# Optimization experiments

Hardware: AMD Instinct MI355X
Metric: run time of the kernel (lower is better)

The kernel has to match this reference:

```python
import jax, jax.numpy as jnp
from jax import lax
import numpy as np

V, D_EMB, H, P, B, T = 32000, 512, 1024, 512, 32, 512
NUM_LAYERS = 2


def setup_inputs() -> dict:
    key = jax.random.key(0)
    ks = jax.random.split(key, 2 + NUM_LAYERS * 5)
    tokens = jax.random.randint(ks[0], (B, T), 0, V, dtype=jnp.int32)
    embed = jax.random.normal(ks[1], (V, D_EMB), dtype=jnp.float32) * 0.02
    inp = {"tokens": tokens, "embed": embed}
    in_dims = [D_EMB] + [P] * (NUM_LAYERS - 1)
    for l in range(NUM_LAYERS):
        kk = ks[2 + 5 * l: 7 + 5 * l]
        inp[f"Wx{l}"] = jax.random.normal(kk[0], (in_dims[l], 4 * H), dtype=jnp.float32) * 0.02
        inp[f"Wh{l}"] = jax.random.normal(kk[1], (H, 4 * H), dtype=jnp.float32) * 0.02
        inp[f"b{l}"] = jnp.zeros((4 * H,), dtype=jnp.float32)
        inp[f"Wfc{l}"] = jax.random.normal(kk[3], (H, P), dtype=jnp.float32) * 0.02
        inp[f"bfc{l}"] = jnp.zeros((P,), dtype=jnp.float32)
    return inp


def _lstm(x, Wx, Wh, b):
    # x: [B, T, D] -> [B, T, H]. Keras gate order: i, f, g(cell), o.
    Bsz = x.shape[0]
    h0 = jnp.zeros((Bsz, H), dtype=x.dtype)
    c0 = jnp.zeros((Bsz, H), dtype=x.dtype)

    # Precompute input projection for all timesteps (one big GEMM).
    xz = jnp.einsum('btd,dg->btg', x, Wx) + b  # [B, T, 4H]

    def step(carry, zt):
        h, c = carry
        z = zt + h @ Wh
        i, f, g, o = jnp.split(z, 4, axis=-1)
        c = jax.nn.sigmoid(f) * c + jax.nn.sigmoid(i) * jnp.tanh(g)
        h = jax.nn.sigmoid(o) * jnp.tanh(c)
        return (h, c), h

    _, ys = lax.scan(step, (h0, c0), jnp.swapaxes(xz, 0, 1))  # ys: [T, B, H]
    return jnp.swapaxes(ys, 0, 1)


def reference(tokens, embed, Wx0, Wh0, b0, Wfc0, bfc0, Wx1, Wh1, b1, Wfc1, bfc1):
    # inference path: dropout is identity (training=False), use_softmax=False
    x = embed[tokens]  # [B, T, D_EMB]
    layers = [(Wx0, Wh0, b0, Wfc0, bfc0), (Wx1, Wh1, b1, Wfc1, bfc1)]
    for Wx, Wh, b, Wfc, bfc in layers:
        x = _lstm(x, Wx, Wh, b)
        x = x @ Wfc + bfc  # per-layer dense projection [B, T, P]
    return x
```

## Files before the change

### kernel.cpp

```cpp
#include <hip/hip_runtime.h>
#include <cstdio>
#include <cstdint>

typedef unsigned short u16;
typedef unsigned int u32;
typedef float f32x4 __attribute__((ext_vector_type(4)));
typedef short s16x8 __attribute__((ext_vector_type(8)));
typedef int i32x2 __attribute__((ext_vector_type(2)));

#define DI __device__ __forceinline__

#define BATCH 32
#define SEQT 512
#define HDIM 1024
#define PDIM 512
#define DEMB 512
#define G4H 4096

DI u16 f2bf(float f) {
  u32 u = __float_as_uint(f);
  return (u16)((u + 0x7fffu + ((u >> 16) & 1u)) >> 16);
}
DI float bf2f(u16 h) { return __uint_as_float(((u32)h) << 16); }
DI void split2(float f, u16 &hi, u16 &lo) {
  hi = f2bf(f);
  lo = f2bf(f - bf2f(hi));
}
DI f32x4 mfma16(s16x8 a, s16x8 b, f32x4 c) {
  return __builtin_amdgcn_mfma_f32_16x16x32_bf16(a, b, c, 0, 0, 0);
}
DI void dma16(const void *g, void *l) {
  __builtin_amdgcn_global_load_lds((const __attribute__((address_space(1))) void *)g,
                                   (__attribute__((address_space(3))) void *)l, 16, 0, 0);
}
DI s16x8 ld128_dev(const u16 *p) {
  s16x8 r;
  asm volatile("global_load_dwordx4 %0, %1, off sc1" : "=v"(r) : "v"(p));
  return r;
}
DI i32x2 ld64_dev(const u16 *p) {
  i32x2 r;
  asm volatile("global_load_dwordx2 %0, %1, off sc1" : "=v"(r) : "v"(p));
  return r;
}
DI void st16_dev(u16 *p, u16 v) {
  asm volatile("global_store_short %0, %1, off sc1" ::"v"(p), "v"((u32)v) : "memory");
}
DI void st32_dev(int *p, int v) {
  asm volatile("global_store_dword %0, %1, off sc1" ::"v"(p), "v"(v) : "memory");
}
DI void st64_dev(u16 *p, i32x2 v) {
  asm volatile("global_store_dwordx2 %0, %1, off sc1" ::"v"(p), "v"(v) : "memory");
}
DI u32 sentq(s16x8 v) {
  union U { s16x8 s; u32 d[4]; } u;
  u.s = v;
  u32 b = 0;
#pragma unroll
  for (int i = 0; i < 4; ++i)
    b |= (u32)(((u.d[i] & 0xffffu) == 0xffffu) || ((u.d[i] >> 16) == 0xffffu));
  return b;
}

#if __has_builtin(__builtin_amdgcn_exp2f) && __has_builtin(__builtin_amdgcn_rcpf)
DI float fsig(float x) {
  return __builtin_amdgcn_rcpf(1.f + __builtin_amdgcn_exp2f(-1.4426950408889634f * x));
}
DI float ftanh(float x) {
  return 2.f * __builtin_amdgcn_rcpf(1.f + __builtin_amdgcn_exp2f(-2.8853900817779268f * x)) - 1.f;
}
#else
DI float fsig(float x) { return 1.f / (1.f + expf(-x)); }
DI float ftanh(float x) { return tanhf(x); }
#endif

__global__ void k_gather_pack(const int *__restrict__ tokens, const float *__restrict__ embed,
                              u16 *__restrict__ xhi, u16 *__restrict__ xlo) {
  int idx = blockIdx.x * 256 + threadIdx.x;
  int m = idx >> 6;
  int k8 = (idx & 63) << 3;
  int tok = tokens[m];
  const float *src = embed + (size_t)tok * DEMB + k8;
  float4 a = *(const float4 *)src;
  float4 b = *(const float4 *)(src + 4);
  float v[8] = {a.x, a.y, a.z, a.w, b.x, b.y, b.z, b.w};
  union UV { u16 h[8]; int4 v; };
  UV uh, ul;
#pragma unroll
  for (int j = 0; j < 8; ++j) split2(v[j], uh.h[j], ul.h[j]);
  size_t o = (size_t)m * DEMB + k8;
  *(int4 *)(xhi + o) = uh.v;
  *(int4 *)(xlo + o) = ul.v;
}

__global__ void k_packT(const float *__restrict__ W, u16 *__restrict__ Thi, u16 *__restrict__ Tlo,
                        int K, int N) {
  __shared__ float tile[32][33];
  int n0 = blockIdx.x * 32, k0 = blockIdx.y * 32;
  int tx = threadIdx.x, ty = threadIdx.y;
#pragma unroll
  for (int i = 0; i < 4; ++i) tile[ty + 8 * i][tx] = W[(size_t)(k0 + ty + 8 * i) * N + n0 + tx];
  __syncthreads();
#pragma unroll
  for (int i = 0; i < 4; ++i) {
    int n = ty + 8 * i;
    u16 hi, lo;
    split2(tile[tx][n], hi, lo);
    size_t o = (size_t)(n0 + n) * K + k0 + tx;
    Thi[o] = hi;
    Tlo[o] = lo;
  }
}

__global__ void k_split(const float *__restrict__ W, u16 *__restrict__ hi, u16 *__restrict__ lo,
                        int n) {
  int i = blockIdx.x * 256 + threadIdx.x;
  if (i < n) split2(W[i], hi[i], lo[i]);
}

__global__ void k_beff(const float *__restrict__ bfc0, const float *__restrict__ Wx1,
                       const float *__restrict__ b1, float *__restrict__ beff) {
  int n = blockIdx.x * 256 + threadIdx.x;
  float acc = b1[n];
  for (int j = 0; j < PDIM; ++j) acc += bfc0[j] * Wx1[(size_t)j * G4H + n];
  beff[n] = acc;
}

template <int OM, int SA>
__global__ __launch_bounds__(256, 2) void k_gemm(const u16 *__restrict__ Ahi, const u16 *__restrict__ Alo,
                                                 const u16 *__restrict__ Bhi, const u16 *__restrict__ Blo,
                                                 const float *__restrict__ bias, void *__restrict__ out0,
                                                 int M, int N, int K) {
  __shared__ u16 sP[4][128 * 64];
  const int tid = threadIdx.x;
  const int w = tid >> 6, lane = tid & 63;
  const int la15 = lane & 15, la4 = lane >> 4;
  const int nbn = N >> 7;
  const int bm = blockIdx.x / nbn, bn = blockIdx.x % nbn;
  const u16 *src = (w == 0) ? Ahi : (w == 1) ? Alo : (w == 2) ? Bhi : Blo;
  const int rowbase = (w < 2) ? bm * 128 : bn * 128;
  char *lds = (char *)&sP[w][0];

  if (SA) {
    for (int i = tid; i < 2048; i += 256) ((unsigned long long *)&sP[1][0])[i] = 0ULL;
  }

  f32x4 acc[2][8] = {};
  for (int kb = 0; kb < K; kb += 64) {
    if (!(SA && w == 1)) {
#pragma unroll
      for (int i = 0; i < 16; ++i) {
        int s = i * 64 + lane;
        int row = s >> 3;
        int k16 = (s & 7) ^ (row & 7);
        dma16(src + (size_t)(rowbase + row) * K + kb + k16 * 8, lds + i * 1024);
      }
    }
    asm volatile("s_waitcnt vmcnt(0)" ::: "memory");
    __syncthreads();
#pragma unroll
    for (int ksl = 0; ksl < 2; ++ksl) {
      s16x8 ah[2], al[2];
#pragma unroll
      for (int rf = 0; rf < 2; ++rf) {
        int row = 32 * w + 16 * rf + la15;
        int slot = row * 8 + ((4 * ksl + la4) ^ (row & 7));
        ah[rf] = *(const s16x8 *)((const char *)&sP[0][0] + slot * 16);
        al[rf] = *(const s16x8 *)((const char *)&sP[1][0] + slot * 16);
      }
#pragma unroll
      for (int cf = 0; cf < 8; ++cf) {
        int col = 16 * cf + la15;
        int slot = col * 8 + ((4 * ksl + la4) ^ (col & 7));
        s16x8 bh = *(const s16x8 *)((const char *)&sP[2][0] + slot * 16);
        s16x8 bl = *(const s16x8 *)((const char *)&sP[3][0] + slot * 16);
#pragma unroll
        for (int rf = 0; rf < 2; ++rf) {
          acc[rf][cf] = mfma16(ah[rf], bh, acc[rf][cf]);
          acc[rf][cf] = mfma16(ah[rf], bl, acc[rf][cf]);
          acc[rf][cf] = mfma16(al[rf], bh, acc[rf][cf]);
        }
      }
    }
    __syncthreads();
  }
#pragma unroll
  for (int rf = 0; rf < 2; ++rf) {
#pragma unroll
    for (int cf = 0; cf < 8; ++cf) {
      int c = bn * 128 + 16 * cf + la15;
      float bv = bias ? bias[c] : 0.f;
#pragma unroll
      for (int q = 0; q < 4; ++q) {
        int r = bm * 128 + 32 * w + 16 * rf + 4 * la4 + q;
        float v = acc[rf][cf][q] + bv;
        if (OM == 0) {
          ((u16 *)out0)[(size_t)r * N + c] = f2bf(v);
        } else {
          int b2 = r & 31, tt = r >> 5;
          ((float *)out0)[((size_t)b2 * SEQT + tt) * PDIM + c] = v;
        }
      }
    }
  }
}

__global__ __launch_bounds__(256, 1) void k_recur_pipe(
    const u16 *__restrict__ xz0, const float *__restrict__ Wh0, const float *__restrict__ Wh1,
    const u16 *__restrict__ Weff, const float *__restrict__ beff,
    u16 *h0h, u16 *h1h, u16 *zeffR, int *flags) {
  __shared__ u16 sW[32 * 1024];
  __shared__ u16 sE[32 * 1024];
  __shared__ float zacc[4][32][33];
  __shared__ float sC[256];
  const int tid = threadIdx.x;
  const int w = tid >> 6, lane = tid & 63;
  const int la15 = lane & 15, la4 = lane >> 4;
  const int wg = blockIdx.x;
  const int layer = wg >> 7;
  const int g = wg & 127;

  const float *Wh = layer ? Wh1 : Wh0;
  for (int i2 = tid; i2 < 32 * 1024; i2 += 256) {
    int zc = i2 & 31;
    int k = i2 >> 5;
    int gcol = (zc >> 3) * HDIM + 8 * g + (zc & 7);
    int boff = zc * 2048 + ((((k >> 3) ^ (zc & 7))) << 4) + (k & 7) * 2;
    *(u16 *)((char *)sW + boff) = f2bf(Wh[(size_t)k * G4H + gcol]);
    if (!layer) *(u16 *)((char *)sE + boff) = Weff[(size_t)k * G4H + gcol];
  }
  sC[tid] = 0.f;
  __syncthreads();

  const int r_g = tid >> 3, hc = tid & 7;
  const int ks0 = 8 * w;

  if (!layer) {
    for (int t = 0; t <= SEQT; ++t) {
      const bool last = (t == SEQT);
      float xzv[4] = {0.f, 0.f, 0.f, 0.f};
      if (!last) {
        const u16 *px = xz0 + ((size_t)r_g * SEQT + t) * G4H + 8 * g + hc;
#pragma unroll
        for (int gi = 0; gi < 4; ++gi) xzv[gi] = bf2f(px[(size_t)gi * HDIM]);
      }
      if (w == 0 && (t & 7) == 0 && t >= 26) {
        const int *f1 = flags + 128 + lane;
        const int bp = t - 25;
        for (long tries = 0;; ++tries) {
          int c = __hip_atomic_load(f1, __ATOMIC_RELAXED, __HIP_MEMORY_SCOPE_AGENT);
          int d = __hip_atomic_load(f1 + 64, __ATOMIC_RELAXED, __HIP_MEMORY_SCOPE_AGENT);
          if (__all(c >= bp && d >= bp)) break;
          if (tries > (1L << 22)) break;
          __builtin_amdgcn_s_sleep(1);
        }
      }
      f32x4 accE[2][2] = {};
      if (t > 0) {
        const u16 *pA = h0h + (size_t)(t - 1) * 32 * HDIM;
        s16x8 aw0[8], aw1[8];
        for (long tries = 0;; ++tries) {
#pragma unroll
          for (int j8 = 0; j8 < 8; ++j8)
            aw0[j8] = ld128_dev(pA + (size_t)la15 * HDIM + 32 * (ks0 + j8) + 8 * la4);
#pragma unroll
          for (int j8 = 0; j8 < 8; ++j8)
            aw1[j8] = ld128_dev(pA + (size_t)(16 + la15) * HDIM + 32 * (ks0 + j8) + 8 * la4);
          asm volatile("s_waitcnt vmcnt(0)" ::: "memory");
          __builtin_amdgcn_sched_barrier(0);
          u32 bad = 0;
#pragma unroll
          for (int j8 = 0; j8 < 8; ++j8) bad |= sentq(aw0[j8]) | sentq(aw1[j8]);
          if (__all(bad == 0)) break;
          if (tries > (1L << 17)) break;
          __builtin_amdgcn_s_sleep(2);
        }
        {
          f32x4 acc0[2] = {};
#pragma unroll
          for (int j8 = 0; j8 < 8; ++j8) {
#pragma unroll
            for (int cf = 0; cf < 2; ++cf) {
              int zc = 16 * cf + la15;
              int sl = (4 * (ks0 + j8) + la4) ^ (zc & 7);
              int boff = zc * 2048 + (sl << 4);
              if (!last) acc0[cf] = mfma16(aw0[j8], *(const s16x8 *)((const char *)sW + boff), acc0[cf]);
              accE[0][cf] = mfma16(aw0[j8], *(const s16x8 *)((const char *)sE + boff), accE[0][cf]);
            }
          }
          if (!last) {
#pragma unroll
            for (int cf = 0; cf < 2; ++cf)
#pragma unroll
              for (int q = 0; q < 4; ++q) zacc[w][4 * la4 + q][16 * cf + la15] = acc0[cf][q];
          }
        }
        {
          f32x4 acc0[2] = {};
#pragma unroll
          for (int j8 = 0; j8 < 8; ++j8) {
#pragma unroll
            for (int cf = 0; cf < 2; ++cf) {
              int zc = 16 * cf + la15;
              int sl = (4 * (ks0 + j8) + la4) ^ (zc & 7);
              int boff = zc * 2048 + (sl << 4);
              if (!last) acc0[cf] = mfma16(aw1[j8], *(const s16x8 *)((const char *)sW + boff), acc0[cf]);
              accE[1][cf] = mfma16(aw1[j8], *(const s16x8 *)((const char *)sE + boff), accE[1][cf]);
            }
          }
          if (!last) {
#pragma unroll
            for (int cf = 0; cf < 2; ++cf)
#pragma unroll
              for (int q = 0; q < 4; ++q) zacc[w][16 + 4 * la4 + q][16 * cf + la15] = acc0[cf][q];
          }
        }
      }
      __syncthreads();
      if (!last) {
        float z4[4];
#pragma unroll
        for (int gi = 0; gi < 4; ++gi) {
          float s = xzv[gi];
          if (t > 0) {
            int zc = gi * 8 + hc;
            s += zacc[0][r_g][zc] + zacc[1][r_g][zc] + zacc[2][r_g][zc] + zacc[3][r_g][zc];
          }
          z4[gi] = s;
        }
        float ig = fsig(z4[0]);
        float fg = fsig(z4[1]);
        float gg = ftanh(z4[2]);
        float og = fsig(z4[3]);
        float c = fg * sC[tid] + ig * gg;
        sC[tid] = c;
        float h = og * ftanh(c);
        st16_dev(h0h + ((size_t)t * 32 + r_g) * HDIM + 8 * g + hc, f2bf(h));
      }
      __syncthreads();
      if (t > 0) {
#pragma unroll
        for (int rt = 0; rt < 2; ++rt)
#pragma unroll
          for (int cf = 0; cf < 2; ++cf)
#pragma unroll
            for (int q = 0; q < 4; ++q)
              zacc[w][16 * rt + 4 * la4 + q][16 * cf + la15] = accE[rt][cf][q];
      }
      __syncthreads();
      if (t > 0) {
        float ze[4];
#pragma unroll
        for (int gi = 0; gi < 4; ++gi) {
          int zc = gi * 8 + hc;
          ze[gi] = zacc[0][r_g][zc] + zacc[1][r_g][zc] + zacc[2][r_g][zc] + zacc[3][r_g][zc];
        }
        i32x2 pk;
        pk[0] = (int)(((u32)f2bf(ze[1]) << 16) | (u32)f2bf(ze[0]));
        pk[1] = (int)(((u32)f2bf(ze[3]) << 16) | (u32)f2bf(ze[2]));
        st64_dev(zeffR + (((size_t)((t - 1) & 31) * 128 + g) << 10) + tid * 4, pk);
      }
      asm volatile("s_waitcnt vmcnt(0)" ::: "memory");
      __syncthreads();
      if (tid == 0) st32_dev(flags + g, t + 1);
    }
  } else {
    float bef[4];
#pragma unroll
    for (int gi = 0; gi < 4; ++gi) bef[gi] = beff[gi * HDIM + 8 * g + hc];
    for (int t = 0; t < SEQT; ++t) {
      s16x8 aw0[8], aw1[8];
      const u16 *pA = h1h + ((t > 0) ? (size_t)(t - 1) * 32 * HDIM : 0);
      if (t > 0) {
#pragma unroll
        for (int j8 = 0; j8 < 8; ++j8)
          aw0[j8] = ld128_dev(pA + (size_t)la15 * HDIM + 32 * (ks0 + j8) + 8 * la4);
#pragma unroll
        for (int j8 = 0; j8 < 8; ++j8)
          aw1[j8] = ld128_dev(pA + (size_t)(16 + la15) * HDIM + 32 * (ks0 + j8) + 8 * la4);
      }
      {
        const int *f0 = flags + lane;
        const int need0 = t + 2;
        for (long tries = 0;; ++tries) {
          int a = __hip_atomic_load(f0, __ATOMIC_RELAXED, __HIP_MEMORY_SCOPE_AGENT);
          int b = __hip_atomic_load(f0 + 64, __ATOMIC_RELAXED, __HIP_MEMORY_SCOPE_AGENT);
          if (__all(a >= need0 && b >= need0)) break;
          if (tries > (1L << 22)) break;
          __builtin_amdgcn_s_sleep(1);
        }
      }
      i32x2 zpk = ld64_dev(zeffR + (((size_t)(t & 31) * 128 + g) << 10) + tid * 4);
      asm volatile("s_waitcnt vmcnt(0)" ::: "memory");
      __builtin_amdgcn_sched_barrier(0);
      float zv[4];
      zv[0] = bf2f((u16)((u32)zpk[0] & 0xffffu));
      zv[1] = bf2f((u16)((u32)zpk[0] >> 16));
      zv[2] = bf2f((u16)((u32)zpk[1] & 0xffffu));
      zv[3] = bf2f((u16)((u32)zpk[1] >> 16));
      if (t > 0) {
        for (long tries = 0;; ++tries) {
          u32 bad = 0;
#pragma unroll
          for (int j8 = 0; j8 < 8; ++j8) bad |= sentq(aw0[j8]) | sentq(aw1[j8]);
          if (__all(bad == 0)) break;
          if (tries > (1L << 17)) break;
          __builtin_amdgcn_s_sleep(2);
#pragma unroll
          for (int j8 = 0; j8 < 8; ++j8)
            aw0[j8] = ld128_dev(pA + (size_t)la15 * HDIM + 32 * (ks0 + j8) + 8 * la4);
#pragma unroll
          for (int j8 = 0; j8 < 8; ++j8)
            aw1[j8] = ld128_dev(pA + (size_t)(16 + la15) * HDIM + 32 * (ks0 + j8) + 8 * la4);
          asm volatile("s_waitcnt vmcnt(0)" ::: "memory");
          __builtin_amdgcn_sched_barrier(0);
        }
        {
          f32x4 acc0[2] = {};
#pragma unroll
          for (int j8 = 0; j8 < 8; ++j8) {
#pragma unroll
            for (int cf = 0; cf < 2; ++cf) {
              int zc = 16 * cf + la15;
              int sl = (4 * (ks0 + j8) + la4) ^ (zc & 7);
              int boff = zc * 2048 + (sl << 4);
              acc0[cf] = mfma16(aw0[j8], *(const s16x8 *)((const char *)sW + boff), acc0[cf]);
            }
          }
#pragma unroll
          for (int cf = 0; cf < 2; ++cf)
#pragma unroll
            for (int q = 0; q < 4; ++q) zacc[w][4 * la4 + q][16 * cf + la15] = acc0[cf][q];
        }
        {
          f32x4 acc0[2] = {};
#pragma unroll
          for (int j8 = 0; j8 < 8; ++j8) {
#pragma unroll
            for (int cf = 0; cf < 2; ++cf) {
              int zc = 16 * cf + la15;
              int sl = (4 * (ks0 + j8) + la4) ^ (zc & 7);
              int boff = zc * 2048 + (sl << 4);
              acc0[cf] = mfma16(aw1[j8], *(const s16x8 *)((const char *)sW + boff), acc0[cf]);
            }
          }
#pragma unroll
          for (int cf = 0; cf < 2; ++cf)
#pragma unroll
            for (int q = 0; q < 4; ++q) zacc[w][16 + 4 * la4 + q][16 * cf + la15] = acc0[cf][q];
        }
      }
      __syncthreads();
      if (tid == 0) st32_dev(flags + 128 + g, t + 1);
      {
        float z4[4];
#pragma unroll
        for (int gi = 0; gi < 4; ++gi) {
          float s = bef[gi] + zv[gi];
          if (t > 0) {
            int zc = gi * 8 + hc;
            s += zacc[0][r_g][zc] + zacc[1][r_g][zc] + zacc[2][r_g][zc] + zacc[3][r_g][zc];
          }
          z4[gi] = s;
        }
        float ig = fsig(z4[0]);
        float fg = fsig(z4[1]);
        float gg = ftanh(z4[2]);
        float og = fsig(z4[3]);
        float c = fg * sC[tid] + ig * gg;
        sC[tid] = c;
        float h = og * ftanh(c);
        st16_dev(h1h + ((size_t)t * 32 + r_g) * HDIM + 8 * g + hc, f2bf(h));
      }
      __syncthreads();
    }
  }
}

extern "C" void kernel_launch(void *const *d_in, const int *in_sizes, int n_in,
                              void *d_out, int out_size, void *d_ws, size_t ws_size,
                              hipStream_t stream) {
  const int *tokens = (const int *)d_in[0];
  const float *embed = (const float *)d_in[1];
  const float *Wx0 = (const float *)d_in[2];
  const float *Wh0 = (const float *)d_in[3];
  const float *b0 = (const float *)d_in[4];
  const float *Wfc0 = (const float *)d_in[5];
  const float *bfc0 = (const float *)d_in[6];
  const float *Wx1 = (const float *)d_in[7];
  const float *Wh1 = (const float *)d_in[8];
  const float *b1 = (const float *)d_in[9];
  const float *Wfc1 = (const float *)d_in[10];
  const float *bfc1 = (const float *)d_in[11];

  constexpr size_t NEED = 255856640;
  if (ws_size < NEED) {
    fprintf(stderr, "RNNLM kernel: ws too small (%zu < %zu)\n", ws_size, NEED);
    return;
  }
  char *ws = (char *)d_ws;
  u16 *xz0 = (u16 *)(ws + 0);
  u16 *h0h = (u16 *)(ws + 134217728);
  u16 *h1h = (u16 *)(ws + 167772160);
  u16 *x0hi = (u16 *)(ws + 201326592);
  u16 *x0lo = (u16 *)(ws + 218103808);
  u16 *Weff = (u16 *)(ws + 201326592);
  u16 *Wfc0hi = (u16 *)(ws + 209715200);
  u16 *Wfc0lo = (u16 *)(ws + 210763776);
  u16 *WfcT1hi = (u16 *)(ws + 211812352);
  u16 *WfcT1lo = (u16 *)(ws + 212860928);
  float *beff = (float *)(ws + 213909504);
  int *flags = (int *)(ws + 213925888);
  u16 *zeffR = (u16 *)(ws + 218103808);
  u16 *WxT0hi = (u16 *)(ws + 234881024);
  u16 *WxT0lo = (u16 *)(ws + 239075328);
  u16 *WxT1hi = (u16 *)(ws + 243269632);
  u16 *WxT1lo = (u16 *)(ws + 247463936);

  (void)hipMemsetAsync(h0h, 0xFF, 67108864, stream);

  k_packT<<<dim3(G4H / 32, DEMB / 32), dim3(32, 8), 0, stream>>>(Wx0, WxT0hi, WxT0lo, DEMB, G4H);
  k_packT<<<dim3(G4H / 32, DEMB / 32), dim3(32, 8), 0, stream>>>(Wx1, WxT1hi, WxT1lo, DEMB, G4H);
  k_gather_pack<<<4096, 256, 0, stream>>>(tokens, embed, x0hi, x0lo);
  k_gemm<0, 0><<<dim3(128 * 32), 256, 0, stream>>>(x0hi, x0lo, WxT0hi, WxT0lo, b0, xz0,
                                                   16384, G4H, DEMB);
  k_split<<<2048, 256, 0, stream>>>(Wfc0, Wfc0hi, Wfc0lo, HDIM * PDIM);
  k_packT<<<dim3(PDIM / 32, HDIM / 32), dim3(32, 8), 0, stream>>>(Wfc1, WfcT1hi, WfcT1lo, HDIM, PDIM);
  k_beff<<<16, 256, 0, stream>>>(bfc0, Wx1, b1, beff);
  (void)hipMemsetAsync(flags, 0, 256 * sizeof(int), stream);
  k_gemm<0, 0><<<dim3(8 * 32), 256, 0, stream>>>(Wfc0hi, Wfc0lo, WxT1hi, WxT1lo, nullptr, Weff,
                                                 1024, G4H, PDIM);
  {
    const u16 *a0 = xz0; const float *a1 = Wh0; const float *a2 = Wh1;
    const u16 *a3 = Weff; const float *a4 = beff;
    u16 *a5 = h0h; u16 *a6 = h1h; u16 *a7 = zeffR; int *a8 = flags;
    void *args[] = {&a0, &a1, &a2, &a3, &a4, &a5, &a6, &a7, &a8};
    hipError_t e = hipLaunchCooperativeKernel((void *)k_recur_pipe, dim3(256), dim3(256), args, 0, stream);
    if (e != hipSuccess) fprintf(stderr, "coop launch failed: %d\n", (int)e);
  }
  k_gemm<2, 1><<<dim3(128 * 4), 256, 0, stream>>>(h1h, h1h, WfcT1hi, WfcT1lo, bfc1, d_out,
                                                  16384, PDIM, HDIM);
}
```

Measured before the change: 4.916 ms.

## Double recurrent block to 512 threads, reduce partials with LDS atomics

The persistent recurrence kernel now runs 8 waves per block instead of 4, so each wave covers half the K slice of the per-step h@Wh and h@Weff products. Per-wave partial accumulators are combined with LDS atomicAdd into single zacc0/zaccE buffers rather than a 4-way split buffer summed by the elementwise threads. This removes two barriers per layer-0 step. The cell state moves from shared memory into a register. The intent is to shorten the per-step serial latency of the recurrence, at the cost of LDS atomic contention and extra zeroing of the buffers each step.

```diff
diff --git a/kernel.cpp b/kernel.cpp
--- a/kernel.cpp
+++ b/kernel.cpp
@@ -205,14 +205,14 @@
   }
 }
 
-__global__ __launch_bounds__(256, 1) void k_recur_pipe(
+__global__ __launch_bounds__(512, 1) void k_recur_pipe(
     const u16 *__restrict__ xz0, const float *__restrict__ Wh0, const float *__restrict__ Wh1,
     const u16 *__restrict__ Weff, const float *__restrict__ beff,
     u16 *h0h, u16 *h1h, u16 *zeffR, int *flags) {
   __shared__ u16 sW[32 * 1024];
   __shared__ u16 sE[32 * 1024];
-  __shared__ float zacc[4][32][33];
-  __shared__ float sC[256];
+  __shared__ float zacc0[32][33];
+  __shared__ float zaccE[32][33];
   const int tid = threadIdx.x;
   const int w = tid >> 6, lane = tid & 63;
   const int la15 = lane & 15, la4 = lane >> 4;
@@ -221,7 +221,7 @@
   const int g = wg & 127;
 
   const float *Wh = layer ? Wh1 : Wh0;
-  for (int i2 = tid; i2 < 32 * 1024; i2 += 256) {
+  for (int i2 = tid; i2 < 32 * 1024; i2 += 512) {
     int zc = i2 & 31;
     int k = i2 >> 5;
     int gcol = (zc >> 3) * HDIM + 8 * g + (zc & 7);
@@ -229,17 +229,24 @@
     *(u16 *)((char *)sW + boff) = f2bf(Wh[(size_t)k * G4H + gcol]);
     if (!layer) *(u16 *)((char *)sE + boff) = Weff[(size_t)k * G4H + gcol];
   }
-  sC[tid] = 0.f;
+  const int r_g = tid >> 3, hc = tid & 7;
+  if (tid < 256) {
+#pragma unroll
+    for (int gi = 0; gi < 4; ++gi) {
+      zacc0[r_g][gi * 8 + hc] = 0.f;
+      zaccE[r_g][gi * 8 + hc] = 0.f;
+    }
+  }
+  float creg = 0.f;
   __syncthreads();
 
-  const int r_g = tid >> 3, hc = tid & 7;
-  const int ks0 = 8 * w;
+  const int ks0 = 4 * w;
 
   if (!layer) {
     for (int t = 0; t <= SEQT; ++t) {
       const bool last = (t == SEQT);
       float xzv[4] = {0.f, 0.f, 0.f, 0.f};
-      if (!last) {
+      if (!last && tid < 256) {
         const u16 *px = xz0 + ((size_t)r_g * SEQT + t) * G4H + 8 * g + hc;
 #pragma unroll
         for (int gi = 0; gi < 4; ++gi) xzv[gi] = bf2f(px[(size_t)gi * HDIM]);
@@ -255,131 +262,104 @@
           __builtin_amdgcn_s_sleep(1);
         }
       }
-      f32x4 accE[2][2] = {};
       if (t > 0) {
         const u16 *pA = h0h + (size_t)(t - 1) * 32 * HDIM;
-        s16x8 aw0[8], aw1[8];
+        s16x8 aw0[4], aw1[4];
         for (long tries = 0;; ++tries) {
 #pragma unroll
-          for (int j8 = 0; j8 < 8; ++j8)
+          for (int j8 = 0; j8 < 4; ++j8)
             aw0[j8] = ld128_dev(pA + (size_t)la15 * HDIM + 32 * (ks0 + j8) + 8 * la4);
 #pragma unroll
-          for (int j8 = 0; j8 < 8; ++j8)
+          for (int j8 = 0; j8 < 4; ++j8)
             aw1[j8] = ld128_dev(pA + (size_t)(16 + la15) * HDIM + 32 * (ks0 + j8) + 8 * la4);
           asm volatile("s_waitcnt vmcnt(0)" ::: "memory");
           __builtin_amdgcn_sched_barrier(0);
           u32 bad = 0;
 #pragma unroll
-          for (int j8 = 0; j8 < 8; ++j8) bad |= sentq(aw0[j8]) | sentq(aw1[j8]);
+          for (int j8 = 0; j8 < 4; ++j8) bad |= sentq(aw0[j8]) | sentq(aw1[j8]);
           if (__all(bad == 0)) break;
           if (tries > (1L << 17)) break;
           __builtin_amdgcn_s_sleep(2);
         }
-        {
-          f32x4 acc0[2] = {};
-#pragma unroll
-          for (int j8 = 0; j8 < 8; ++j8) {
+#pragma unroll
+        for (int rt = 0; rt < 2; ++rt) {
+          f32x4 acc0[2] = {}, accE[2] = {};
+#pragma unroll
+          for (int j8 = 0; j8 < 4; ++j8) {
+            s16x8 a = rt ? aw1[j8] : aw0[j8];
 #pragma unroll
             for (int cf = 0; cf < 2; ++cf) {
               int zc = 16 * cf + la15;
               int sl = (4 * (ks0 + j8) + la4) ^ (zc & 7);
               int boff = zc * 2048 + (sl << 4);
-              if (!last) acc0[cf] = mfma16(aw0[j8], *(const s16x8 *)((const char *)sW + boff), acc0[cf]);
-              accE[0][cf] = mfma16(aw0[j8], *(const s16x8 *)((const char *)sE + boff), accE[0][cf]);
+              if (!last) acc0[cf] = mfma16(a, *(const s16x8 *)((const char *)sW + boff), acc0[cf]);
+              accE[cf] = mfma16(a, *(const s16x8 *)((const char *)sE + boff), accE[cf]);
             }
           }
-          if (!last) {
-#pragma unroll
-            for (int cf = 0; cf < 2; ++cf)
-#pragma unroll
-              for (int q = 0; q < 4; ++q) zacc[w][4 * la4 + q][16 * cf + la15] = acc0[cf][q];
-          }
-        }
-        {
-          f32x4 acc0[2] = {};
-#pragma unroll
-          for (int j8 = 0; j8 < 8; ++j8) {
-#pragma unroll
-            for (int cf = 0; cf < 2; ++cf) {
-              int zc = 16 * cf + la15;
-              int sl = (4 * (ks0 + j8) + la4) ^ (zc & 7);
-              int boff = zc * 2048 + (sl << 4);
-              if (!last) acc0[cf] = mfma16(aw1[j8], *(const s16x8 *)((const char *)sW + boff), acc0[cf]);
-              accE[1][cf] = mfma16(aw1[j8], *(const s16x8 *)((const char *)sE + boff), accE[1][cf]);
+#pragma unroll
+          for (int cf = 0; cf < 2; ++cf) {
+            int zc = 16 * cf + la15;
+#pragma unroll
+            for (int q = 0; q < 4; ++q) {
+              int row = 16 * rt + 4 * la4 + q;
+              if (!last) atomicAdd(&zacc0[row][zc], acc0[cf][q]);
+              atomicAdd(&zaccE[row][zc], accE[cf][q]);
             }
           }
-          if (!last) {
-#pragma unroll
-            for (int cf = 0; cf < 2; ++cf)
-#pragma unroll
-              for (int q = 0; q < 4; ++q) zacc[w][16 + 4 * la4 + q][16 * cf + la15] = acc0[cf][q];
-          }
         }
       }
       __syncthreads();
-      if (!last) {
-        float z4[4];
+      if (tid < 256) {
+        if (!last) {
+          float z4[4];
+#pragma unroll
+          for (int gi = 0; gi < 4; ++gi) z4[gi] = xzv[gi] + zacc0[r_g][gi * 8 + hc];
+          float ig = fsig(z4[0]);
+          float fg = fsig(z4[1]);
+          float gg = ftanh(z4[2]);
+          float og = fsig(z4[3]);
+          creg = fg * creg + ig * gg;
+          float h = og * ftanh(creg);
+          st16_dev(h0h + ((size_t)t * 32 + r_g) * HDIM + 8 * g + hc, f2bf(h));
+        }
+        if (t > 0) {
+          float ze[4];
+#pragma unroll
+          for (int gi = 0; gi < 4; ++gi) ze[gi] = zaccE[r_g][gi * 8 + hc];
+          i32x2 pk;
+          pk[0] = (int)(((u32)f2bf(ze[1]) << 16) | (u32)f2bf(ze[0]));
+          pk[1] = (int)(((u32)f2bf(ze[3]) << 16) | (u32)f2bf(ze[2]));
+          st64_dev(zeffR + (((size_t)((t - 1) & 31) * 128 + g) << 10) + tid * 4, pk);
+        }
 #pragma unroll
         for (int gi = 0; gi < 4; ++gi) {
-          float s = xzv[gi];
-          if (t > 0) {
-            int zc = gi * 8 + hc;
-            s += zacc[0][r_g][zc] + zacc[1][r_g][zc] + zacc[2][r_g][zc] + zacc[3][r_g][zc];
-          }
-          z4[gi] = s;
-        }
-        float ig = fsig(z4[0]);
-        float fg = fsig(z4[1]);
-        float gg = ftanh(z4[2]);
-        float og = fsig(z4[3]);
-        float c = fg * sC[tid] + ig * gg;
-        sC[tid] = c;
-        float h = og * ftanh(c);
-        st16_dev(h0h + ((size_t)t * 32 + r_g) * HDIM + 8 * g + hc, f2bf(h));
-      }
-      __syncthreads();
-      if (t > 0) {
-#pragma unroll
-        for (int rt = 0; rt < 2; ++rt)
-#pragma unroll
-          for (int cf = 0; cf < 2; ++cf)
-#pragma unroll
-            for (int q = 0; q < 4; ++q)
-              zacc[w][16 * rt + 4 * la4 + q][16 * cf + la15] = accE[rt][cf][q];
-      }
-      __syncthreads();
-      if (t > 0) {
-        float ze[4];
-#pragma unroll
-        for (int gi = 0; gi < 4; ++gi) {
-          int zc = gi * 8 + hc;
-          ze[gi] = zacc[0][r_g][zc] + zacc[1][r_g][zc] + zacc[2][r_g][zc] + zacc[3][r_g][zc];
-        }
-        i32x2 pk;
-        pk[0] = (int)(((u32)f2bf(ze[1]) << 16) | (u32)f2bf(ze[0]));
-        pk[1] = (int)(((u32)f2bf(ze[3]) << 16) | (u32)f2bf(ze[2]));
-        st64_dev(zeffR + (((size_t)((t - 1) & 31) * 128 + g) << 10) + tid * 4, pk);
-      }
-      asm volatile("s_waitcnt vmcnt(0)" ::: "memory");
+          zacc0[r_g][gi * 8 + hc] = 0.f;
+          zaccE[r_g][gi * 8 + hc] = 0.f;
+        }
+        asm volatile("s_waitcnt vmcnt(0)" ::: "memory");
+      }
       __syncthreads();
       if (tid == 0) st32_dev(flags + g, t + 1);
     }
   } else {
-    float bef[4];
-#pragma unroll
-    for (int gi = 0; gi < 4; ++gi) bef[gi] = beff[gi * HDIM + 8 * g + hc];
+    float bef[4] = {0.f, 0.f, 0.f, 0.f};
+    if (tid < 256) {
+#pragma unroll
+      for (int gi = 0; gi < 4; ++gi) bef[gi] = beff[gi * HDIM + 8 * g + hc];
+    }
     for (int t = 0; t < SEQT; ++t) {
-      s16x8 aw0[8], aw1[8];
+      s16x8 aw0[4], aw1[4];
       const u16 *pA = h1h + ((t > 0) ? (size_t)(t - 1) * 32 * HDIM : 0);
       if (t > 0) {
 #pragma unroll
-        for (int j8 = 0; j8 < 8; ++j8)
+        for (int j8 = 0; j8 < 4; ++j8)
           aw0[j8] = ld128_dev(pA + (size_t)la15 * HDIM + 32 * (ks0 + j8) + 8 * la4);
 #pragma unroll
-        for (int j8 = 0; j8 < 8; ++j8)
+        for (int j8 = 0; j8 < 4; ++j8)
           aw1[j8] = ld128_dev(pA + (size_t)(16 + la15) * HDIM + 32 * (ks0 + j8) + 8 * la4);
       }
-      {
+      float zv[4] = {0.f, 0.f, 0.f, 0.f};
+      if (w < 4) {
         const int *f0 = flags + lane;
         const int need0 = t + 2;
         for (long tries = 0;; ++tries) {
@@ -389,88 +369,73 @@
           if (tries > (1L << 22)) break;
           __builtin_amdgcn_s_sleep(1);
         }
-      }
-      i32x2 zpk = ld64_dev(zeffR + (((size_t)(t & 31) * 128 + g) << 10) + tid * 4);
-      asm volatile("s_waitcnt vmcnt(0)" ::: "memory");
-      __builtin_amdgcn_sched_barrier(0);
-      float zv[4];
-      zv[0] = bf2f((u16)((u32)zpk[0] & 0xffffu));
-      zv[1] = bf2f((u16)((u32)zpk[0] >> 16));
-      zv[2] = bf2f((u16)((u32)zpk[1] & 0xffffu));
-      zv[3] = bf2f((u16)((u32)zpk[1] >> 16));
+        i32x2 zpk = ld64_dev(zeffR + (((size_t)(t & 31) * 128 + g) << 10) + tid * 4);
+        asm volatile("s_waitcnt vmcnt(0)" ::: "memory");
+        __builtin_amdgcn_sched_barrier(0);
+        zv[0] = bf2f((u16)((u32)zpk[0] & 0xffffu));
+        zv[1] = bf2f((u16)((u32)zpk[0] >> 16));
+        zv[2] = bf2f((u16)((u32)zpk[1] & 0xffffu));
+        zv[3] = bf2f((u16)((u32)zpk[1] >> 16));
+      } else if (t > 0) {
+        asm volatile("s_waitcnt vmcnt(0)" ::: "memory");
+        __builtin_amdgcn_sched_barrier(0);
+      }
       if (t > 0) {
         for (long tries = 0;; ++tries) {
           u32 bad = 0;
 #pragma unroll
-          for (int j8 = 0; j8 < 8; ++j8) bad |= sentq(aw0[j8]) | sentq(aw1[j8]);
+          for (int j8 = 0; j8 < 4; ++j8) bad |= sentq(aw0[j8]) | sentq(aw1[j8]);
           if (__all(bad == 0)) break;
           if (tries > (1L << 17)) break;
           __builtin_amdgcn_s_sleep(2);
 #pragma unroll
-          for (int j8 = 0; j8 < 8; ++j8)
+          for (int j8 = 0; j8 < 4; ++j8)
             aw0[j8] = ld128_dev(pA + (size_t)la15 * HDIM + 32 * (ks0 + j8) + 8 * la4);
 #pragma unroll
-          for (int j8 = 0; j8 < 8; ++j8)
+          for (int j8 = 0; j8 < 4; ++j8)
             aw1[j8] = ld128_dev(pA + (size_t)(16 + la15) * HDIM + 32 * (ks0 + j8) + 8 * la4);
           asm volatile("s_waitcnt vmcnt(0)" ::: "memory");
           __builtin_amdgcn_sched_barrier(0);
         }
-        {
+#pragma unroll
+        for (int rt = 0; rt < 2; ++rt) {
           f32x4 acc0[2] = {};
 #pragma unroll
-          for (int j8 = 0; j8 < 8; ++j8) {
+          for (int j8 = 0; j8 < 4; ++j8) {
+            s16x8 a = rt ? aw1[j8] : aw0[j8];
 #pragma unroll
             for (int cf = 0; cf < 2; ++cf) {
               int zc = 16 * cf + la15;
               int sl = (4 * (ks0 + j8) + la4) ^ (zc & 7);
               int boff = zc * 2048 + (sl << 4);
-              acc0[cf] = mfma16(aw0[j8], *(const s16x8 *)((const char *)sW + boff), acc0[cf]);
+              acc0[cf] = mfma16(a, *(const s16x8 *)((const char *)sW + boff), acc0[cf]);
             }
           }
 #pragma unroll
-          for (int cf = 0; cf < 2; ++cf)
-#pragma unroll
-            for (int q = 0; q < 4; ++q) zacc[w][4 * la4 + q][16 * cf + la15] = acc0[cf][q];
-        }
-        {
-          f32x4 acc0[2] = {};
-#pragma unroll
-          for (int j8 = 0; j8 < 8; ++j8) {
-#pragma unroll
-            for (int cf = 0; cf < 2; ++cf) {
-              int zc = 16 * cf + la15;
-              int sl = (4 * (ks0 + j8) + la4) ^ (zc & 7);
-              int boff = zc * 2048 + (sl << 4);
-              acc0[cf] = mfma16(aw1[j8], *(const s16x8 *)((const char *)sW + boff), acc0[cf]);
-            }
+          for (int cf = 0; cf < 2; ++cf) {
+            int zc = 16 * cf + la15;
+#pragma unroll
+            for (int q = 0; q < 4; ++q)
+              atomicAdd(&zacc0[16 * rt + 4 * la4 + q][zc], acc0[cf][q]);
           }
-#pragma unroll
-          for (int cf = 0; cf < 2; ++cf)
-#pragma unroll
-            for (int q = 0; q < 4; ++q) zacc[w][16 + 4 * la4 + q][16 * cf + la15] = acc0[cf][q];
         }
       }
       __syncthreads();
       if (tid == 0) st32_dev(flags + 128 + g, t + 1);
-      {
+      if (tid < 256) {
         float z4[4];
 #pragma unroll
-        for (int gi = 0; gi < 4; ++gi) {
-          float s = bef[gi] + zv[gi];
-          if (t > 0) {
-            int zc = gi * 8 + hc;
-            s += zacc[0][r_g][zc] + zacc[1][r_g][zc] + zacc[2][r_g][zc] + zacc[3][r_g][zc];
-          }
-          z4[gi] = s;
-        }
+        for (int gi = 0; gi < 4; ++gi)
+          z4[gi] = bef[gi] + zv[gi] + zacc0[r_g][gi * 8 + hc];
         float ig = fsig(z4[0]);
         float fg = fsig(z4[1]);
         float gg = ftanh(z4[2]);
         float og = fsig(z4[3]);
-        float c = fg * sC[tid] + ig * gg;
-        sC[tid] = c;
-        float h = og * ftanh(c);
+        creg = fg * creg + ig * gg;
+        float h = og * ftanh(creg);
         st16_dev(h1h + ((size_t)t * 32 + r_g) * HDIM + 8 * g + hc, f2bf(h));
+#pragma unroll
+        for (int gi = 0; gi < 4; ++gi) zacc0[r_g][gi * 8 + hc] = 0.f;
       }
       __syncthreads();
     }
@@ -535,7 +500,7 @@
     const u16 *a3 = Weff; const float *a4 = beff;
     u16 *a5 = h0h; u16 *a6 = h1h; u16 *a7 = zeffR; int *a8 = flags;
     void *args[] = {&a0, &a1, &a2, &a3, &a4, &a5, &a6, &a7, &a8};
-    hipError_t e = hipLaunchCooperativeKernel((void *)k_recur_pipe, dim3(256), dim3(256), args, 0, stream);
+    hipError_t e = hipLaunchCooperativeKernel((void *)k_recur_pipe, dim3(256), dim3(512), args, 0, stream);
     if (e != hipSuccess) fprintf(stderr, "coop launch failed: %d\n", (int)e);
   }
   k_gemm<2, 1><<<dim3(128 * 4), 256, 0, stream>>>(h1h, h1h, WfcT1hi, WfcT1lo, bfc1, d_out,
```

Result: slower. 14.10 ms (+186.9%).

## Move layer-1 input partial-sum reduction into consumer, drop two producer barriers

Applied to the files above, without the earlier changes.

The layer-0 producer no longer reduces the four per-wave partial products of Weff·h through shared memory before publishing them. Each wave writes its own bf16 partials directly to the ring buffer, which removes two __syncthreads and one LDS round trip from the serial critical path of layer 0. The layer-1 consumer now loads four partials, sums them and scatters the result through a new shared array. The ring depth shrinks from 32 to 16 and the backpressure wait threshold is tightened to match. In exchange the global traffic per step is four times larger, and because each partial is rounded to bf16 before summing, the results may differ slightly in precision.

```diff
diff --git a/kernel.cpp b/kernel.cpp
--- a/kernel.cpp
+++ b/kernel.cpp
@@ -212,6 +212,7 @@
   __shared__ u16 sW[32 * 1024];
   __shared__ u16 sE[32 * 1024];
   __shared__ float zacc[4][32][33];
+  __shared__ float zE[32][33];
   __shared__ float sC[256];
   const int tid = threadIdx.x;
   const int w = tid >> 6, lane = tid & 63;
@@ -244,9 +245,9 @@
 #pragma unroll
         for (int gi = 0; gi < 4; ++gi) xzv[gi] = bf2f(px[(size_t)gi * HDIM]);
       }
-      if (w == 0 && (t & 7) == 0 && t >= 26) {
+      if (w == 0 && (t & 7) == 0 && t >= 16) {
         const int *f1 = flags + 128 + lane;
-        const int bp = t - 25;
+        const int bp = t - 9;
         for (long tries = 0;; ++tries) {
           int c = __hip_atomic_load(f1, __ATOMIC_RELAXED, __HIP_MEMORY_SCOPE_AGENT);
           int d = __hip_atomic_load(f1 + 64, __ATOMIC_RELAXED, __HIP_MEMORY_SCOPE_AGENT);
@@ -255,7 +256,6 @@
           __builtin_amdgcn_s_sleep(1);
         }
       }
-      f32x4 accE[2][2] = {};
       if (t > 0) {
         const u16 *pA = h0h + (size_t)(t - 1) * 32 * HDIM;
         s16x8 aw0[8], aw1[8];
@@ -275,44 +275,33 @@
           if (tries > (1L << 17)) break;
           __builtin_amdgcn_s_sleep(2);
         }
-        {
-          f32x4 acc0[2] = {};
+        u16 *zb = zeffR + ((((size_t)((t - 1) & 15) * 128 + g) << 12) + (w << 10));
+#pragma unroll
+        for (int rt = 0; rt < 2; ++rt) {
+          f32x4 acc0[2] = {}, accE[2] = {};
 #pragma unroll
           for (int j8 = 0; j8 < 8; ++j8) {
+            s16x8 a = rt ? aw1[j8] : aw0[j8];
 #pragma unroll
             for (int cf = 0; cf < 2; ++cf) {
               int zc = 16 * cf + la15;
               int sl = (4 * (ks0 + j8) + la4) ^ (zc & 7);
               int boff = zc * 2048 + (sl << 4);
-              if (!last) acc0[cf] = mfma16(aw0[j8], *(const s16x8 *)((const char *)sW + boff), acc0[cf]);
-              accE[0][cf] = mfma16(aw0[j8], *(const s16x8 *)((const char *)sE + boff), accE[0][cf]);
+              if (!last) acc0[cf] = mfma16(a, *(const s16x8 *)((const char *)sW + boff), acc0[cf]);
+              accE[cf] = mfma16(a, *(const s16x8 *)((const char *)sE + boff), accE[cf]);
             }
           }
-          if (!last) {
-#pragma unroll
-            for (int cf = 0; cf < 2; ++cf)
-#pragma unroll
-              for (int q = 0; q < 4; ++q) zacc[w][4 * la4 + q][16 * cf + la15] = acc0[cf][q];
-          }
-        }
-        {
-          f32x4 acc0[2] = {};
-#pragma unroll
-          for (int j8 = 0; j8 < 8; ++j8) {
-#pragma unroll
-            for (int cf = 0; cf < 2; ++cf) {
-              int zc = 16 * cf + la15;
-              int sl = (4 * (ks0 + j8) + la4) ^ (zc & 7);
-              int boff = zc * 2048 + (sl << 4);
-              if (!last) acc0[cf] = mfma16(aw1[j8], *(const s16x8 *)((const char *)sW + boff), acc0[cf]);
-              accE[1][cf] = mfma16(aw1[j8], *(const s16x8 *)((const char *)sE + boff), accE[1][cf]);
+#pragma unroll
+          for (int cf = 0; cf < 2; ++cf) {
+            if (!last) {
+#pragma unroll
+              for (int q = 0; q < 4; ++q)
+                zacc[w][16 * rt + 4 * la4 + q][16 * cf + la15] = acc0[cf][q];
             }
-          }
-          if (!last) {
-#pragma unroll
-            for (int cf = 0; cf < 2; ++cf)
-#pragma unroll
-              for (int q = 0; q < 4; ++q) zacc[w][16 + 4 * la4 + q][16 * cf + la15] = acc0[cf][q];
+            i32x2 pk;
+            pk[0] = (int)(((u32)f2bf(accE[cf][1]) << 16) | (u32)f2bf(accE[cf][0]));
+            pk[1] = (int)(((u32)f2bf(accE[cf][3]) << 16) | (u32)f2bf(accE[cf][2]));
+            st64_dev(zb + ((rt * 2 + cf) << 8) + (lane << 2), pk);
           }
         }
       }
@@ -337,29 +326,6 @@
         float h = og * ftanh(c);
         st16_dev(h0h + ((size_t)t * 32 + r_g) * HDIM + 8 * g + hc, f2bf(h));
       }
-      __syncthreads();
-      if (t > 0) {
-#pragma unroll
-        for (int rt = 0; rt < 2; ++rt)
-#pragma unroll
-          for (int cf = 0; cf < 2; ++cf)
-#pragma unroll
-            for (int q = 0; q < 4; ++q)
-              zacc[w][16 * rt + 4 * la4 + q][16 * cf + la15] = accE[rt][cf][q];
-      }
-      __syncthreads();
-      if (t > 0) {
-        float ze[4];
-#pragma unroll
-        for (int gi = 0; gi < 4; ++gi) {
-          int zc = gi * 8 + hc;
-          ze[gi] = zacc[0][r_g][zc] + zacc[1][r_g][zc] + zacc[2][r_g][zc] + zacc[3][r_g][zc];
-        }
-        i32x2 pk;
-        pk[0] = (int)(((u32)f2bf(ze[1]) << 16) | (u32)f2bf(ze[0]));
-        pk[1] = (int)(((u32)f2bf(ze[3]) << 16) | (u32)f2bf(ze[2]));
-        st64_dev(zeffR + (((size_t)((t - 1) & 31) * 128 + g) << 10) + tid * 4, pk);
-      }
       asm volatile("s_waitcnt vmcnt(0)" ::: "memory");
       __syncthreads();
       if (tid == 0) st32_dev(flags + g, t + 1);
@@ -368,6 +334,7 @@
     float bef[4];
 #pragma unroll
     for (int gi = 0; gi < 4; ++gi) bef[gi] = beff[gi * HDIM + 8 * g + hc];
+    const int rtL = w >> 1, cfL = w & 1;
     for (int t = 0; t < SEQT; ++t) {
       s16x8 aw0[8], aw1[8];
       const u16 *pA = h1h + ((t > 0) ? (size_t)(t - 1) * 32 * HDIM : 0);
@@ -390,14 +357,28 @@
           __builtin_amdgcn_s_sleep(1);
         }
       }
-      i32x2 zpk = ld64_dev(zeffR + (((size_t)(t & 31) * 128 + g) << 10) + tid * 4);
+      const u16 *rb = zeffR + ((((size_t)(t & 15) * 128 + g) << 12) + (w << 8) + (lane << 2));
+      i32x2 zp0 = ld64_dev(rb);
+      i32x2 zp1 = ld64_dev(rb + 1024);
+      i32x2 zp2 = ld64_dev(rb + 2048);
+      i32x2 zp3 = ld64_dev(rb + 3072);
       asm volatile("s_waitcnt vmcnt(0)" ::: "memory");
       __builtin_amdgcn_sched_barrier(0);
-      float zv[4];
-      zv[0] = bf2f((u16)((u32)zpk[0] & 0xffffu));
-      zv[1] = bf2f((u16)((u32)zpk[0] >> 16));
-      zv[2] = bf2f((u16)((u32)zpk[1] & 0xffffu));
-      zv[3] = bf2f((u16)((u32)zpk[1] >> 16));
+      {
+        float s0 = bf2f((u16)((u32)zp0[0] & 0xffffu)) + bf2f((u16)((u32)zp1[0] & 0xffffu)) +
+                   bf2f((u16)((u32)zp2[0] & 0xffffu)) + bf2f((u16)((u32)zp3[0] & 0xffffu));
+        float s1 = bf2f((u16)((u32)zp0[0] >> 16)) + bf2f((u16)((u32)zp1[0] >> 16)) +
+                   bf2f((u16)((u32)zp2[0] >> 16)) + bf2f((u16)((u32)zp3[0] >> 16));
+        float s2 = bf2f((u16)((u32)zp0[1] & 0xffffu)) + bf2f((u16)((u32)zp1[1] & 0xffffu)) +
+                   bf2f((u16)((u32)zp2[1] & 0xffffu)) + bf2f((u16)((u32)zp3[1] & 0xffffu));
+        float s3 = bf2f((u16)((u32)zp0[1] >> 16)) + bf2f((u16)((u32)zp1[1] >> 16)) +
+                   bf2f((u16)((u32)zp2[1] >> 16)) + bf2f((u16)((u32)zp3[1] >> 16));
+        int zcL = 16 * cfL + la15, rowL = 16 * rtL + 4 * la4;
+        zE[rowL + 0][zcL] = s0;
+        zE[rowL + 1][zcL] = s1;
+        zE[rowL + 2][zcL] = s2;
+        zE[rowL + 3][zcL] = s3;
+      }
       if (t > 0) {
         for (long tries = 0;; ++tries) {
           u32 bad = 0;
@@ -415,39 +396,25 @@
           asm volatile("s_waitcnt vmcnt(0)" ::: "memory");
           __builtin_amdgcn_sched_barrier(0);
         }
-        {
+#pragma unroll
+        for (int rt = 0; rt < 2; ++rt) {
           f32x4 acc0[2] = {};
 #pragma unroll
           for (int j8 = 0; j8 < 8; ++j8) {
+            s16x8 a = rt ? aw1[j8] : aw0[j8];
 #pragma unroll
             for (int cf = 0; cf < 2; ++cf) {
               int zc = 16 * cf + la15;
               int sl = (4 * (ks0 + j8) + la4) ^ (zc & 7);
               int boff = zc * 2048 + (sl << 4);
-              acc0[cf] = mfma16(aw0[j8], *(const s16x8 *)((const char *)sW + boff), acc0[cf]);
+              acc0[cf] = mfma16(a, *(const s16x8 *)((const char *)sW + boff), acc0[cf]);
             }
           }
 #pragma unroll
           for (int cf = 0; cf < 2; ++cf)
 #pragma unroll
-            for (int q = 0; q < 4; ++q) zacc[w][4 * la4 + q][16 * cf + la15] = acc0[cf][q];
-        }
-        {
-          f32x4 acc0[2] = {};
-#pragma unroll
-          for (int j8 = 0; j8 < 8; ++j8) {
-#pragma unroll
-            for (int cf = 0; cf < 2; ++cf) {
-              int zc = 16 * cf + la15;
-              int sl = (4 * (ks0 + j8) + la4) ^ (zc & 7);
-              int boff = zc * 2048 + (sl << 4);
-              acc0[cf] = mfma16(aw1[j8], *(const s16x8 *)((const char *)sW + boff), acc0[cf]);
-            }
-          }
-#pragma unroll
-          for (int cf = 0; cf < 2; ++cf)
-#pragma unroll
-            for (int q = 0; q < 4; ++q) zacc[w][16 + 4 * la4 + q][16 * cf + la15] = acc0[cf][q];
+            for (int q = 0; q < 4; ++q)
+              zacc[w][16 * rt + 4 * la4 + q][16 * cf + la15] = acc0[cf][q];
         }
       }
       __syncthreads();
@@ -456,11 +423,10 @@
         float z4[4];
 #pragma unroll
         for (int gi = 0; gi < 4; ++gi) {
-          float s = bef[gi] + zv[gi];
-          if (t > 0) {
-            int zc = gi * 8 + hc;
+          int zc = gi * 8 + hc;
+          float s = bef[gi] + zE[r_g][zc];
+          if (t > 0)
             s += zacc[0][r_g][zc] + zacc[1][r_g][zc] + zacc[2][r_g][zc] + zacc[3][r_g][zc];
-          }
           z4[gi] = s;
         }
         float ig = fsig(z4[0]);
```

New measurement: 4.862 ms, median of 2. No clear change (-1.1%).
